# Performance work log

Measured on AMD Instinct MI355X. Metric: run time of the kernel, lower is better.

Reference implementation:

```python
import jax, jax.numpy as jnp
import numpy as np

NUM_VIEWS = 6
NUM_HEADS = 16
NUM_LAYERS = 2
DIST_THRESHOLD = 10.0
EPS = 1e-5


def layer_norm(x, g, b):
    m = jnp.mean(x, axis=-1, keepdims=True)
    v = jnp.mean((x - m) ** 2, axis=-1, keepdims=True)
    return (x - m) / jnp.sqrt(v + EPS) * g + b


def build_mask(coords3d, num_views, threshold):
    # coords3d: (B, T, 3) -> bool mask (B, T, T), True = masked
    B, T, _ = coords3d.shape
    tpv = T // num_views
    c = jnp.nan_to_num(coords3d, nan=0.0, posinf=100.0, neginf=-100.0)
    view_ids = jnp.repeat(jnp.arange(num_views), tpv)
    same_view = view_ids[:, None] == view_ids[None, :]  # (T, T)
    dist_sq = jnp.sum((c[:, :, None, :] - c[:, None, :, :]) ** 2, axis=-1)  # (B,T,T)
    mask = same_view[None] | (dist_sq > threshold * threshold)
    all_masked = jnp.all(mask, axis=-1)  # (B, T)
    eye = jnp.eye(T, dtype=bool)
    # unmask diagonal for rows that are fully masked (matches torch fix)
    mask = jnp.where(all_masked[:, :, None] & eye[None], False, mask)
    return mask


def mha(x, qkv_w, qkv_b, out_w, out_b, mask, num_heads):
    # x: (B,T,C); qkv_w: (3C,C); out_w: (C,C); mask: (B,T,T) True=masked
    B, T, C = x.shape
    hd = C // num_heads
    qkv = x @ qkv_w.T + qkv_b  # (B,T,3C)
    q, k, v = jnp.split(qkv, 3, axis=-1)
    def heads(t):
        return t.reshape(B, T, num_heads, hd).transpose(0, 2, 1, 3)  # (B,H,T,hd)
    q, k, v = heads(q), heads(k), heads(v)
    scale = 1.0 / jnp.sqrt(jnp.asarray(hd, x.dtype))
    scores = jnp.einsum('bhqd,bhkd->bhqk', q * scale, k)
    scores = jnp.where(mask[:, None], -jnp.inf, scores)
    attn = jax.nn.softmax(scores, axis=-1)
    o = jnp.einsum('bhqk,bhkd->bhqd', attn, v)  # (B,H,T,hd)
    o = o.transpose(0, 2, 1, 3).reshape(B, T, C)
    return o @ out_w.T + out_b


def setup_inputs() -> dict:
    key = jax.random.key(0)
    B, T, C, L = 2, 1536, 1024, NUM_LAYERS
    ks = jax.random.split(key, 16)
    s = 0.02
    inp = {
        'pos_embed': jax.random.normal(ks[0], (B, T, C), jnp.float32),
        'coords3d': jax.random.normal(ks[1], (B, T, 3), jnp.float32) * 8.0,
        'ln1_g': jnp.ones((L, C), jnp.float32),
        'ln1_b': jnp.zeros((L, C), jnp.float32),
        'qkv_w': jax.random.normal(ks[2], (L, 3 * C, C), jnp.float32) * s,
        'qkv_b': jnp.zeros((L, 3 * C), jnp.float32),
        'out_w': jax.random.normal(ks[3], (L, C, C), jnp.float32) * s,
        'out_b': jnp.zeros((L, C), jnp.float32),
        'ln2_g': jnp.ones((L, C), jnp.float32),
        'ln2_b': jnp.zeros((L, C), jnp.float32),
        'ffn_w1': jax.random.normal(ks[4], (L, 4 * C, C), jnp.float32) * s,
        'ffn_b1': jnp.zeros((L, 4 * C), jnp.float32),
        'ffn_w2': jax.random.normal(ks[5], (L, C, 4 * C), jnp.float32) * s,
        'ffn_b2': jnp.zeros((L, C), jnp.float32),
        'norm_g': jnp.ones((C,), jnp.float32),
        'norm_b': jnp.zeros((C,), jnp.float32),
    }
    return inp


def reference(pos_embed, coords3d, ln1_g, ln1_b, qkv_w, qkv_b, out_w, out_b,
              ln2_g, ln2_b, ffn_w1, ffn_b1, ffn_w2, ffn_b2, norm_g, norm_b):
    mask = build_mask(coords3d, NUM_VIEWS, DIST_THRESHOLD)
    x = pos_embed
    for l in range(NUM_LAYERS):
        xn = layer_norm(x, ln1_g[l], ln1_b[l])
        x = x + mha(xn, qkv_w[l], qkv_b[l], out_w[l], out_b[l], mask, NUM_HEADS)
        xn = layer_norm(x, ln2_g[l], ln2_b[l])
        h = jax.nn.gelu(xn @ ffn_w1[l].T + ffn_b1[l], approximate=False)
        x = x + (h @ ffn_w2[l].T + ffn_b2[l])
    return layer_norm(x, norm_g, norm_b)
```

## Files before the change

### kernel.cpp

```cpp
#include <hip/hip_runtime.h>

#define TT 1536
#define CC 1024
#define NH 16
#define HD 64
#define NL 2
#define NB 2
#define MM (NB*TT)

typedef unsigned short u16;
typedef unsigned int u32;
typedef unsigned long long u64;
typedef __attribute__((ext_vector_type(8))) short short8v;
typedef __attribute__((ext_vector_type(4))) float f32x4;

__device__ __forceinline__ u16 f2bf(float f){
  u32 u = __float_as_uint(f);
  u32 r = (u + 0x7FFFu + ((u >> 16) & 1u)) >> 16;
  return (u16)r;
}

__device__ __forceinline__ void gload_lds16(const void* g, void* l){
  __builtin_amdgcn_global_load_lds(
      (const __attribute__((address_space(1))) void*)g,
      (__attribute__((address_space(3))) void*)l, 16, 0, 0);
}

__device__ __forceinline__ f32x4 mfma16(short8v a, short8v b, f32x4 c){
  return __builtin_amdgcn_mfma_f32_16x16x32_bf16(a, b, c, 0, 0, 0);
}

__device__ __forceinline__ float exp2f_fast(float x){
  return __builtin_amdgcn_exp2f(x);
}

__device__ __forceinline__ u32 cvt_pk_bf16(float lo, float hi){
  u32 r;
  asm("v_cvt_pk_bf16_f32 %0, %1, %2" : "=v"(r) : "v"(lo), "v"(hi));
  return r;
}

__global__ __launch_bounds__(256) void cvt_bf16_kernel(const float* __restrict__ in,
                                                       u16* __restrict__ out, int n4){
  int stride = gridDim.x * 256;
  for (int i = blockIdx.x * 256 + threadIdx.x; i < n4; i += stride){
    const float4 v = ((const float4*)in)[i];
    ushort4 o;
    o.x = f2bf(v.x); o.y = f2bf(v.y); o.z = f2bf(v.z); o.w = f2bf(v.w);
    ((ushort4*)out)[i] = o;
  }
}

__device__ __forceinline__ float fixc(float v){
  if (__builtin_isnan(v)) return 0.0f;
  if (__builtin_isinf(v)) return v > 0.0f ? 100.0f : -100.0f;
  return v;
}

__global__ __launch_bounds__(256) void mask_kernel(const float* __restrict__ coords,
                                                   u64* __restrict__ maskw){
  const int tid = threadIdx.x, wave = tid >> 6, lane = tid & 63;
  const int ri = blockIdx.x * 4 + wave;
  const int b = ri / TT, i = ri - b * TT;
  const float* cp = coords + (size_t)ri * 3;
  const float cx = fixc(cp[0]), cy = fixc(cp[1]), cz = fixc(cp[2]);
  const int vi = i >> 8;
  u64 allm = ~0ull;
  for (int ch = 0; ch < 24; ++ch){
    const int j = ch * 64 + lane;
    const float* cj = coords + ((size_t)b * TT + j) * 3;
    const float dx = cx - fixc(cj[0]);
    const float dy = cy - fixc(cj[1]);
    const float dz = cz - fixc(cj[2]);
    const float d2 = dx*dx + dy*dy + dz*dz;
    const bool masked = ((j >> 8) == vi) || (d2 > 100.0f);
    const u64 bal = __ballot(masked);
    if (lane == 0) maskw[(size_t)ri * 24 + ch] = bal;
    allm &= bal;
  }
  if (lane == 0 && allm == ~0ull){
    const size_t w = (size_t)ri * 24 + (i >> 6);
    maskw[w] &= ~(1ull << (i & 63));
  }
}

template<int OUTF>
__global__ __launch_bounds__(256) void ln_kernel(const float* __restrict__ x,
    const float* __restrict__ gw, const float* __restrict__ bw,
    u16* __restrict__ outb, float* __restrict__ outf){
  __shared__ float sred[4];
  const int tid = threadIdx.x, wave = tid >> 6, lane = tid & 63;
  const size_t row = blockIdx.x;
  const float4 v = *(const float4*)(x + row * CC + tid * 4);
  float s = v.x + v.y + v.z + v.w;
  #pragma unroll
  for (int o = 1; o < 64; o <<= 1) s += __shfl_xor(s, o, 64);
  if (lane == 0) sred[wave] = s;
  __syncthreads();
  const float mean = (sred[0] + sred[1] + sred[2] + sred[3]) * (1.0f / CC);
  __syncthreads();
  const float d0 = v.x - mean, d1 = v.y - mean, d2 = v.z - mean, d3 = v.w - mean;
  float q = d0*d0 + d1*d1 + d2*d2 + d3*d3;
  #pragma unroll
  for (int o = 1; o < 64; o <<= 1) q += __shfl_xor(q, o, 64);
  if (lane == 0) sred[wave] = q;
  __syncthreads();
  const float var = (sred[0] + sred[1] + sred[2] + sred[3]) * (1.0f / CC);
  const float rstd = rsqrtf(var + 1e-5f);
  const float4 g4 = *(const float4*)(gw + tid * 4);
  const float4 b4 = *(const float4*)(bw + tid * 4);
  const float y0 = d0 * rstd * g4.x + b4.x;
  const float y1 = d1 * rstd * g4.y + b4.y;
  const float y2 = d2 * rstd * g4.z + b4.z;
  const float y3 = d3 * rstd * g4.w + b4.w;
  if (OUTF){
    *(float4*)(outf + row * CC + tid * 4) = make_float4(y0, y1, y2, y3);
  } else {
    ushort4 o4; o4.x = f2bf(y0); o4.y = f2bf(y1); o4.z = f2bf(y2); o4.w = f2bf(y3);
    *(ushort4*)(outb + row * CC + tid * 4) = o4;
  }
}

template<int EPI, int BM>
__global__ __launch_bounds__(512, 4) void gemm_nt(const u16* __restrict__ A,
    const u16* __restrict__ Bw, const float* __restrict__ bias,
    const float* __restrict__ res, u16* __restrict__ outb, float* __restrict__ outf,
    int M, int N, int K){
  __shared__ u16 As[2][BM][64];
  __shared__ u16 Bs[2][128][64];
  const int tid = threadIdx.x, wave = tid >> 6, lane = tid & 63;
  const int gx = gridDim.x;
  const int nwg = gx * gridDim.y;
  const int orig = blockIdx.y * gx + blockIdx.x;
  const int qq = nwg >> 3, rm = nwg & 7;
  const int xcd = orig & 7, pos = orig >> 3;
  const int wg = (xcd < rm ? xcd * (qq + 1) : rm * (qq + 1) + (xcd - rm) * qq) + pos;
  const int m0 = (wg / gx) * BM, n0 = (wg % gx) * 128;
  constexpr int NFR = (BM == 128) ? 4 : 2;
  constexpr int CW = 16 * NFR;
  const int wr = (BM == 128) ? (wave >> 1) : (wave >> 2);
  const int wc = (BM == 128) ? (wave & 1) : (wave & 3);
  f32x4 acc[2][NFR];
  #pragma unroll
  for (int mi = 0; mi < 2; ++mi)
    #pragma unroll
    for (int ni = 0; ni < NFR; ++ni){ f32x4 z = {0.f,0.f,0.f,0.f}; acc[mi][ni] = z; }

  const u16* Ag = A + (size_t)m0 * K;
  const u16* Bg = Bw + (size_t)n0 * K;
  const int srow0 = wave * 8 + (lane >> 3);
  const int scole = ((lane & 7) ^ (lane >> 3)) * 8;
  auto stage = [&](int buf, int k0){
    char* ab = (char*)&As[buf][0][0];
    char* bb = (char*)&Bs[buf][0][0];
    #pragma unroll
    for (int l = 0; l < BM/64; ++l)
      gload_lds16(Ag + (size_t)(l*64 + srow0) * K + k0 + scole, ab + (l*8 + wave) * 1024);
    #pragma unroll
    for (int l = 0; l < 2; ++l)
      gload_lds16(Bg + (size_t)(l*64 + srow0) * K + k0 + scole, bb + (l*8 + wave) * 1024);
  };

  const int NT = K >> 6;
  stage(0, 0);
  stage(1, 64);

  const int ar = lane & 15, akb = (lane >> 4) * 16;
  const int rsw = (ar & 7) << 4;
  for (int t = 0; t < NT; ++t){
    const int cur = t & 1;
    if (t + 1 < NT){
      if constexpr (BM == 128) asm volatile("s_waitcnt vmcnt(4)" ::: "memory");
      else                     asm volatile("s_waitcnt vmcnt(3)" ::: "memory");
    } else {
      asm volatile("s_waitcnt vmcnt(0)" ::: "memory");
    }
    __builtin_amdgcn_s_barrier();
    const char* ab = (const char*)&As[cur][0][0];
    const char* bb = (const char*)&Bs[cur][0][0];
    short8v af[2][2], bf[NFR][2];
    #pragma unroll
    for (int ks = 0; ks < 2; ++ks){
      const int cb = (ks*64 + akb) ^ rsw;
      #pragma unroll
      for (int mi = 0; mi < 2; ++mi)
        af[mi][ks] = *(const short8v*)(ab + (wr*32 + mi*16 + ar)*128 + cb);
      #pragma unroll
      for (int ni = 0; ni < NFR; ++ni)
        bf[ni][ks] = *(const short8v*)(bb + (wc*CW + ni*16 + ar)*128 + cb);
    }
    asm volatile("s_waitcnt lgkmcnt(0)" ::: "memory");
    __builtin_amdgcn_sched_barrier(0);
    __builtin_amdgcn_s_barrier();
    if (t + 2 < NT) stage(cur, (t + 2) * 64);
    __builtin_amdgcn_s_setprio(1);
    #pragma unroll
    for (int ks = 0; ks < 2; ++ks)
      #pragma unroll
      for (int mi = 0; mi < 2; ++mi)
        #pragma unroll
        for (int ni = 0; ni < NFR; ++ni)
          acc[mi][ni] = mfma16(af[mi][ks], bf[ni][ks], acc[mi][ni]);
    __builtin_amdgcn_s_setprio(0);
  }

  const int cr = (lane >> 4) * 4, cl = lane & 15;
  #pragma unroll
  for (int ni = 0; ni < NFR; ++ni){
    const int c = n0 + wc*CW + ni*16 + cl;
    const float bv = bias[c];
    #pragma unroll
    for (int mi = 0; mi < 2; ++mi){
      #pragma unroll
      for (int r = 0; r < 4; ++r){
        const size_t rr2 = (size_t)(m0 + wr*32 + mi*16 + cr + r);
        float v = acc[mi][ni][r] + bv;
        if constexpr (EPI == 1) v = 0.5f * v * (1.0f + erff(v * 0.70710678118654752f));
        if constexpr (EPI == 2) outf[rr2 * N + c] = v + res[rr2 * N + c];
        else outb[rr2 * N + c] = f2bf(v);
      }
    }
  }
}

__global__ __launch_bounds__(256, 3) void attn_kernel(const u16* __restrict__ qkv,
    const u64* __restrict__ maskw, u16* __restrict__ outp){
  __shared__ u16 Ks[2][64][64];
  __shared__ u16 Vt[2][64][64];
  __shared__ u16 Ps[4][16][64];
  const int tid = threadIdx.x, wave = tid >> 6, lane = tid & 63;
  const int nwgA = gridDim.x * gridDim.y;
  const int flatA = blockIdx.y * gridDim.x + blockIdx.x;
  const int virt = (flatA & 7) * (nwgA >> 3) + (flatA >> 3);
  const int bh = virt / (TT/64);
  const int qt = virt - bh * (TT/64);
  const int b = bh >> 4, h = bh & 15;
  const int qb = qt * 64;
  const int rs = 3 * CC;
  const int g4 = lane >> 4;
  const int l15 = lane & 15;
  const int qrow = qb + wave * 16 + l15;
  const u16* kv_base = qkv + (size_t)b * TT * rs;

  const float qscale = 0.18033688011112042f;
  const u16* qp = kv_base + (size_t)qrow * rs + h * HD + g4 * 8;
  short8v qf0, qf1;
  {
    const short8v r0 = *(const short8v*)qp;
    const short8v r1 = *(const short8v*)(qp + 32);
    #pragma unroll
    for (int e = 0; e < 8; ++e){
      qf0[e] = (short)f2bf(__uint_as_float(((u32)(u16)r0[e]) << 16) * qscale);
      qf1[e] = (short)f2bf(__uint_as_float(((u32)(u16)r1[e]) << 16) * qscale);
    }
  }

  f32x4 o[4], lacc;
  #pragma unroll
  for (int dt = 0; dt < 4; ++dt){ f32x4 z = {0.f,0.f,0.f,0.f}; o[dt] = z; }
  { f32x4 z = {0.f,0.f,0.f,0.f}; lacc = z; }
  float m_r = -1.0e4f;

  const int sw = (l15 & 7) << 4;
  const int swl = (lane & 7) << 4;
  int koff[4][2], voff[4][2], pwoff[4], proff[2], vwoff[2];
  #pragma unroll
  for (int jt = 0; jt < 4; ++jt){
    koff[jt][0] = (jt*16 + l15)*128 + ((g4*16) ^ sw);
    koff[jt][1] = (jt*16 + l15)*128 + ((64 + g4*16) ^ sw);
    voff[jt][0] = koff[jt][0];
    voff[jt][1] = koff[jt][1];
    pwoff[jt] = wave*2048 + l15*128 + ((jt*32 + g4*8) ^ sw);
  }
  proff[0] = wave*2048 + l15*128 + ((g4*16) ^ sw);
  proff[1] = wave*2048 + l15*128 + ((64 + g4*16) ^ sw);
  vwoff[0] = lane*128 + ((wave*16) ^ swl);
  vwoff[1] = lane*128 + ((64 + wave*16) ^ swl);

  const int scol = CC + h * HD + (((lane & 7) ^ (lane >> 3)) * 8);
  const u16* skp0 = kv_base + (size_t)(64 + wave*16 + (lane >> 3)) * rs + scol;
  const u16* skp1 = skp0 + 8 * rs;
  const u16* vp   = kv_base + (size_t)(64 + wave*8) * rs + 2*CC + h*HD + lane;
  const u64* mp2  = maskw + (size_t)(b * TT + qrow) * 24;

  char* KsB = (char*)&Ks[0][0][0];
  char* VtB = (char*)&Vt[0][0][0];
  char* PsB = (char*)&Ps[0][0][0];

  short8v vone;
  #pragma unroll
  for (int e = 0; e < 8; ++e) vone[e] = (short)0x3F80;

  {
    u16 vv[16];
    #pragma unroll
    for (int e = 0; e < 8; ++e)
      vv[e] = kv_base[(size_t)(wave*8 + e) * rs + 2*CC + h*HD + lane];
    #pragma unroll
    for (int e = 0; e < 8; ++e)
      vv[8+e] = kv_base[(size_t)(32 + wave*8 + e) * rs + 2*CC + h*HD + lane];
    gload_lds16(kv_base + (size_t)(wave*16 + (lane>>3)) * rs + scol,
                KsB + (wave*2 + 0) * 1024);
    gload_lds16(kv_base + (size_t)(wave*16 + 8 + (lane>>3)) * rs + scol,
                KsB + (wave*2 + 1) * 1024);
    short8v sv0, sv1;
    #pragma unroll
    for (int e = 0; e < 8; ++e){ sv0[e] = (short)vv[e]; sv1[e] = (short)vv[8+e]; }
    *(short8v*)(VtB + vwoff[0]) = sv0;
    *(short8v*)(VtB + vwoff[1]) = sv1;
    __syncthreads();
  }

  auto chunk = [&](int buf, bool pf){
    u16 vv[16];
    if (pf){
      #pragma unroll
      for (int e = 0; e < 8; ++e) vv[e] = vp[(size_t)e * rs];
      #pragma unroll
      for (int e = 0; e < 8; ++e) vv[8+e] = vp[(size_t)(32 + e) * rs];
      gload_lds16(skp0, KsB + (buf^1)*8192 + (wave*2 + 0)*1024);
      gload_lds16(skp1, KsB + (buf^1)*8192 + (wave*2 + 1)*1024);
    }
    const u64 mw = mp2[buf];
    const u32 mwlo = (u32)mw, mwhi = (u32)(mw >> 32);

    const char* Kb = KsB + buf * 8192;
    f32x4 S[4];
    #pragma unroll
    for (int jt = 0; jt < 4; ++jt){
      const short8v k0 = *(const short8v*)(Kb + koff[jt][0]);
      const short8v k1 = *(const short8v*)(Kb + koff[jt][1]);
      f32x4 z = {0.f,0.f,0.f,0.f};
      z = mfma16(k0, qf0, z);
      z = mfma16(k1, qf1, z);
      S[jt] = z;
    }

    float ps[16];
    float cmax = -3.0e38f;
    #pragma unroll
    for (int jt = 0; jt < 4; ++jt){
      const u32 msrc = (jt & 2) ? mwhi : mwlo;
      const int sh = g4 * 4 + (jt & 1) * 16;
      #pragma unroll
      for (int r = 0; r < 4; ++r){
        float s = S[jt][r];
        s = ((msrc >> (sh + r)) & 1u) ? -3.0e38f : s;
        ps[jt*4+r] = s;
        cmax = fmaxf(cmax, s);
      }
    }
    cmax = fmaxf(cmax, __shfl_xor(cmax, 16));
    cmax = fmaxf(cmax, __shfl_xor(cmax, 32));

    if (!__all(cmax <= m_r + 8.0f)){
      const float mnew = fmaxf(m_r, cmax);
      const float fac = exp2f_fast(m_r - mnew);
      m_r = mnew;
      float fr4[4];
      #pragma unroll
      for (int r = 0; r < 4; ++r) fr4[r] = __shfl(fac, g4 * 4 + r);
      #pragma unroll
      for (int dt = 0; dt < 4; ++dt){
        f32x4 tt = o[dt];
        tt[0] *= fr4[0]; tt[1] *= fr4[1]; tt[2] *= fr4[2]; tt[3] *= fr4[3];
        o[dt] = tt;
      }
      lacc[0] *= fr4[0]; lacc[1] *= fr4[1]; lacc[2] *= fr4[2]; lacc[3] *= fr4[3];
    }

    #pragma unroll
    for (int i = 0; i < 16; ++i) ps[i] = exp2f_fast(ps[i] - m_r);

    #pragma unroll
    for (int jt = 0; jt < 4; ++jt){
      uint2 pk;
      pk.x = cvt_pk_bf16(ps[jt*4+0], ps[jt*4+1]);
      pk.y = cvt_pk_bf16(ps[jt*4+2], ps[jt*4+3]);
      *(uint2*)(PsB + pwoff[jt]) = pk;
    }

    short8v pA[2];
    pA[0] = *(const short8v*)(PsB + proff[0]);
    pA[1] = *(const short8v*)(PsB + proff[1]);
    const char* Vb = VtB + buf * 8192;
    __builtin_amdgcn_s_setprio(1);
    #pragma unroll
    for (int dt = 0; dt < 4; ++dt){
      #pragma unroll
      for (int kc = 0; kc < 2; ++kc){
        const short8v vf = *(const short8v*)(Vb + voff[dt][kc]);
        o[dt] = mfma16(pA[kc], vf, o[dt]);
      }
    }
    lacc = mfma16(pA[0], vone, lacc);
    lacc = mfma16(pA[1], vone, lacc);
    __builtin_amdgcn_s_setprio(0);

    if (pf){
      short8v sv0, sv1;
      #pragma unroll
      for (int e = 0; e < 8; ++e){ sv0[e] = (short)vv[e]; sv1[e] = (short)vv[8+e]; }
      char* Vd = VtB + (buf^1) * 8192;
      *(short8v*)(Vd + vwoff[0]) = sv0;
      *(short8v*)(Vd + vwoff[1]) = sv1;
      vp += (size_t)64 * rs; skp0 += (size_t)64 * rs; skp1 += (size_t)64 * rs;
    }
    __syncthreads();
  };

  for (int th = 0; th < 12; ++th){
    chunk(0, true);
    chunk(1, th < 11);
    mp2 += 2;
  }

  float linv[4];
  #pragma unroll
  for (int r = 0; r < 4; ++r) linv[r] = 1.0f / fmaxf(lacc[r], 1e-30f);
  #pragma unroll
  for (int dt = 0; dt < 4; ++dt)
    #pragma unroll
    for (int r = 0; r < 4; ++r)
      outp[(size_t)(b * TT + qb + wave * 16 + g4 * 4 + r) * CC + h * HD + dt * 16 + l15] =
          f2bf(o[dt][r] * linv[r]);
}

extern "C" void kernel_launch(void* const* d_in, const int* in_sizes, int n_in,
                              void* d_out, int out_size, void* d_ws, size_t ws_size,
                              hipStream_t stream){
  (void)in_sizes; (void)n_in; (void)out_size; (void)ws_size;
  const float* pos    = (const float*)d_in[0];
  const float* coords = (const float*)d_in[1];
  const float* ln1g   = (const float*)d_in[2];
  const float* ln1b   = (const float*)d_in[3];
  const float* qkvw   = (const float*)d_in[4];
  const float* qkvbi  = (const float*)d_in[5];
  const float* outw   = (const float*)d_in[6];
  const float* outbi  = (const float*)d_in[7];
  const float* ln2g   = (const float*)d_in[8];
  const float* ln2b   = (const float*)d_in[9];
  const float* w1     = (const float*)d_in[10];
  const float* b1     = (const float*)d_in[11];
  const float* w2     = (const float*)d_in[12];
  const float* b2     = (const float*)d_in[13];
  const float* ng     = (const float*)d_in[14];
  const float* nbb    = (const float*)d_in[15];

  char* wsp = (char*)d_ws;
  size_t off = 0;
  auto alloc = [&](size_t bytes)->void*{
    void* p = wsp + off; off += (bytes + 255) & ~(size_t)255; return p;
  };
  u16* qkvw_bf = (u16*)alloc((size_t)NL*3*CC*CC*sizeof(u16));
  u16* outw_bf = (u16*)alloc((size_t)NL*CC*CC*sizeof(u16));
  u16* w1_bf   = (u16*)alloc((size_t)NL*4*CC*CC*sizeof(u16));
  u16* w2_bf   = (u16*)alloc((size_t)NL*4*CC*CC*sizeof(u16));
  float* x     = (float*)alloc((size_t)MM*CC*sizeof(float));
  u16* xn      = (u16*)alloc((size_t)MM*CC*sizeof(u16));
  u16* qkvbuf  = (u16*)alloc((size_t)MM*4*CC*sizeof(u16));
  u16* attnb   = (u16*)alloc((size_t)MM*CC*sizeof(u16));
  u64* maskw   = (u64*)alloc((size_t)MM*24*sizeof(u64));
  u16* hbuf = qkvbuf;

  auto cvt = [&](const float* s, u16* dst, size_t n){
    int n4 = (int)(n >> 2);
    int blocks = (n4 + 255) / 256; if (blocks > 4096) blocks = 4096;
    cvt_bf16_kernel<<<dim3(blocks), dim3(256), 0, stream>>>(s, dst, n4);
  };
  cvt(qkvw, qkvw_bf, (size_t)NL*3*CC*CC);
  cvt(outw, outw_bf, (size_t)NL*CC*CC);
  cvt(w1, w1_bf, (size_t)NL*4*CC*CC);
  cvt(w2, w2_bf, (size_t)NL*4*CC*CC);

  hipMemcpyAsync(x, pos, (size_t)MM*CC*sizeof(float), hipMemcpyDeviceToDevice, stream);
  mask_kernel<<<dim3(MM/4), dim3(256), 0, stream>>>(coords, maskw);

  for (int l = 0; l < NL; ++l){
    ln_kernel<0><<<dim3(MM), dim3(256), 0, stream>>>(x, ln1g + l*CC, ln1b + l*CC, xn, nullptr);
    gemm_nt<0,128><<<dim3(3*CC/128, MM/128), dim3(512), 0, stream>>>(
        xn, qkvw_bf + (size_t)l*3*CC*CC, qkvbi + l*3*CC, nullptr, qkvbuf, nullptr, MM, 3*CC, CC);
    attn_kernel<<<dim3(TT/64, NB*NH), dim3(256), 0, stream>>>(qkvbuf, maskw, attnb);
    gemm_nt<2,64><<<dim3(CC/128, MM/64), dim3(512), 0, stream>>>(
        attnb, outw_bf + (size_t)l*CC*CC, outbi + l*CC, x, nullptr, x, MM, CC, CC);
    ln_kernel<0><<<dim3(MM), dim3(256), 0, stream>>>(x, ln2g + l*CC, ln2b + l*CC, xn, nullptr);
    gemm_nt<1,128><<<dim3(4*CC/128, MM/128), dim3(512), 0, stream>>>(
        xn, w1_bf + (size_t)l*4*CC*CC, b1 + l*4*CC, nullptr, hbuf, nullptr, MM, 4*CC, CC);
    gemm_nt<2,64><<<dim3(CC/128, MM/64), dim3(512), 0, stream>>>(
        hbuf, w2_bf + (size_t)l*4*CC*CC, b2 + l*CC, x, nullptr, x, MM, CC, 4*CC);
  }
  ln_kernel<1><<<dim3(MM), dim3(256), 0, stream>>>(x, ng, nbb, nullptr, (float*)d_out);
}
```

Baseline: 425.6 us.

## Add 4-wave 128x128 GEMM with 64x64 per-wave tiles for QKV and FFN1

Adds a 256-thread GEMM variant in which each of four waves computes a 64x64 sub-tile (4x4 MFMA fragments) instead of the 8-wave layout, and uses it for the QKV projection and the first FFN GEMM. The larger per-wave tile raises register-level reuse of the A and B fragments loaded from LDS, cutting LDS read traffic per MFMA. The cost is more accumulator registers and lower occupancy (launch bounds of 2 blocks). The attention kernel's launch bound is also raised from 3 to 4 blocks per CU, which pushes its register budget down and may cause spills.

```diff
diff --git a/kernel.cpp b/kernel.cpp
--- a/kernel.cpp
+++ b/kernel.cpp
@@ -121,6 +121,100 @@
   }
 }
 
+template<int EPI>
+__global__ __launch_bounds__(256, 2) void gemm_nt4(const u16* __restrict__ A,
+    const u16* __restrict__ Bw, const float* __restrict__ bias,
+    const float* __restrict__ res, u16* __restrict__ outb, float* __restrict__ outf,
+    int M, int N, int K){
+  __shared__ u16 As[2][128][64];
+  __shared__ u16 Bs[2][128][64];
+  const int tid = threadIdx.x, wave = tid >> 6, lane = tid & 63;
+  const int gx = gridDim.x;
+  const int nwg = gx * gridDim.y;
+  const int orig = blockIdx.y * gx + blockIdx.x;
+  const int qq = nwg >> 3, rm = nwg & 7;
+  const int xcd = orig & 7, pos = orig >> 3;
+  const int wg = (xcd < rm ? xcd * (qq + 1) : rm * (qq + 1) + (xcd - rm) * qq) + pos;
+  const int m0 = (wg / gx) * 128, n0 = (wg % gx) * 128;
+  const int wr = wave >> 1, wc = wave & 1;
+  f32x4 acc[4][4];
+  #pragma unroll
+  for (int mi = 0; mi < 4; ++mi)
+    #pragma unroll
+    for (int ni = 0; ni < 4; ++ni){ f32x4 z = {0.f,0.f,0.f,0.f}; acc[mi][ni] = z; }
+
+  const u16* Ag = A + (size_t)m0 * K;
+  const u16* Bg = Bw + (size_t)n0 * K;
+  const int srow0 = tid >> 3;
+  const int scole = ((tid & 7) ^ ((tid >> 3) & 7)) * 8;
+  auto stage = [&](int buf, int k0){
+    char* ab = (char*)&As[buf][0][0];
+    char* bb = (char*)&Bs[buf][0][0];
+    #pragma unroll
+    for (int l = 0; l < 4; ++l){
+      gload_lds16(Ag + (size_t)(l*32 + srow0) * K + k0 + scole, ab + l*4096 + tid*16);
+      gload_lds16(Bg + (size_t)(l*32 + srow0) * K + k0 + scole, bb + l*4096 + tid*16);
+    }
+  };
+
+  const int NT = K >> 6;
+  stage(0, 0);
+  stage(1, 64);
+
+  const int ar = lane & 15, akb = (lane >> 4) * 16;
+  const int rsw = (ar & 7) << 4;
+  for (int t = 0; t < NT; ++t){
+    const int cur = t & 1;
+    if (t + 1 < NT) asm volatile("s_waitcnt vmcnt(8)" ::: "memory");
+    else            asm volatile("s_waitcnt vmcnt(0)" ::: "memory");
+    __builtin_amdgcn_s_barrier();
+    const char* ab = (const char*)&As[cur][0][0];
+    const char* bb = (const char*)&Bs[cur][0][0];
+    short8v af[4][2], bf[4][2];
+    #pragma unroll
+    for (int ks = 0; ks < 2; ++ks){
+      const int cb = (ks*64 + akb) ^ rsw;
+      #pragma unroll
+      for (int mi = 0; mi < 4; ++mi)
+        af[mi][ks] = *(const short8v*)(ab + (wr*64 + mi*16 + ar)*128 + cb);
+      #pragma unroll
+      for (int ni = 0; ni < 4; ++ni)
+        bf[ni][ks] = *(const short8v*)(bb + (wc*64 + ni*16 + ar)*128 + cb);
+    }
+    asm volatile("s_waitcnt lgkmcnt(0)" ::: "memory");
+    __builtin_amdgcn_sched_barrier(0);
+    __builtin_amdgcn_s_barrier();
+    if (t + 2 < NT) stage(cur, (t + 2) * 64);
+    __builtin_amdgcn_s_setprio(1);
+    #pragma unroll
+    for (int ks = 0; ks < 2; ++ks)
+      #pragma unroll
+      for (int mi = 0; mi < 4; ++mi)
+        #pragma unroll
+        for (int ni = 0; ni < 4; ++ni)
+          acc[mi][ni] = mfma16(af[mi][ks], bf[ni][ks], acc[mi][ni]);
+    __builtin_amdgcn_s_setprio(0);
+  }
+
+  const int cr = (lane >> 4) * 4, cl = lane & 15;
+  #pragma unroll
+  for (int ni = 0; ni < 4; ++ni){
+    const int c = n0 + wc*64 + ni*16 + cl;
+    const float bv = bias[c];
+    #pragma unroll
+    for (int mi = 0; mi < 4; ++mi){
+      #pragma unroll
+      for (int r = 0; r < 4; ++r){
+        const size_t rr2 = (size_t)(m0 + wr*64 + mi*16 + cr + r);
+        float v = acc[mi][ni][r] + bv;
+        if constexpr (EPI == 1) v = 0.5f * v * (1.0f + erff(v * 0.70710678118654752f));
+        if constexpr (EPI == 2) outf[rr2 * N + c] = v + res[rr2 * N + c];
+        else outb[rr2 * N + c] = f2bf(v);
+      }
+    }
+  }
+}
+
 template<int EPI, int BM>
 __global__ __launch_bounds__(512, 4) void gemm_nt(const u16* __restrict__ A,
     const u16* __restrict__ Bw, const float* __restrict__ bias,
@@ -223,7 +317,7 @@
   }
 }
 
-__global__ __launch_bounds__(256, 3) void attn_kernel(const u16* __restrict__ qkv,
+__global__ __launch_bounds__(256, 4) void attn_kernel(const u16* __restrict__ qkv,
     const u64* __restrict__ maskw, u16* __restrict__ outp){
   __shared__ u16 Ks[2][64][64];
   __shared__ u16 Vt[2][64][64];
@@ -478,13 +572,13 @@
 
   for (int l = 0; l < NL; ++l){
     ln_kernel<0><<<dim3(MM), dim3(256), 0, stream>>>(x, ln1g + l*CC, ln1b + l*CC, xn, nullptr);
-    gemm_nt<0,128><<<dim3(3*CC/128, MM/128), dim3(512), 0, stream>>>(
+    gemm_nt4<0><<<dim3(3*CC/128, MM/128), dim3(256), 0, stream>>>(
         xn, qkvw_bf + (size_t)l*3*CC*CC, qkvbi + l*3*CC, nullptr, qkvbuf, nullptr, MM, 3*CC, CC);
     attn_kernel<<<dim3(TT/64, NB*NH), dim3(256), 0, stream>>>(qkvbuf, maskw, attnb);
     gemm_nt<2,64><<<dim3(CC/128, MM/64), dim3(512), 0, stream>>>(
         attnb, outw_bf + (size_t)l*CC*CC, outbi + l*CC, x, nullptr, x, MM, CC, CC);
     ln_kernel<0><<<dim3(MM), dim3(256), 0, stream>>>(x, ln2g + l*CC, ln2b + l*CC, xn, nullptr);
-    gemm_nt<1,128><<<dim3(4*CC/128, MM/128), dim3(512), 0, stream>>>(
+    gemm_nt4<1><<<dim3(4*CC/128, MM/128), dim3(256), 0, stream>>>(
         xn, w1_bf + (size_t)l*4*CC*CC, b1 + l*4*CC, nullptr, hbuf, nullptr, MM, 4*CC, CC);
     gemm_nt<2,64><<<dim3(CC/128, MM/64), dim3(512), 0, stream>>>(
         hbuf, w2_bf + (size_t)l*4*CC*CC, b2 + l*CC, x, nullptr, x, MM, CC, 4*CC);
```

Measured after the change: 442.7 us. 4.0% more time.

## Store residual stream in bf16 and raise attention occupancy bound

Applied to the files above, without the earlier changes.

The fp32 residual stream x becomes bf16. LayerNorm reads bf16, and the residual GEMM epilogues read and write bf16 instead of fp32. The initial device copy of pos_embed becomes a bf16 conversion kernel. This halves residual read/write traffic in the LN and projection epilogues, at the cost of accumulating rounding error in the residual across layers. The attention kernel's launch bounds also change from 3 to 4 waves-per-SIMD minimum, which may increase register pressure or spills.

```diff
diff --git a/kernel.cpp b/kernel.cpp
--- a/kernel.cpp
+++ b/kernel.cpp
@@ -18,6 +18,10 @@
   u32 u = __float_as_uint(f);
   u32 r = (u + 0x7FFFu + ((u >> 16) & 1u)) >> 16;
   return (u16)r;
+}
+
+__device__ __forceinline__ float b2f(u16 u){
+  return __uint_as_float(((u32)u) << 16);
 }
 
 __device__ __forceinline__ void gload_lds16(const void* g, void* l){
@@ -85,21 +89,22 @@
 }
 
 template<int OUTF>
-__global__ __launch_bounds__(256) void ln_kernel(const float* __restrict__ x,
+__global__ __launch_bounds__(256) void ln_kernel(const u16* __restrict__ x,
     const float* __restrict__ gw, const float* __restrict__ bw,
     u16* __restrict__ outb, float* __restrict__ outf){
   __shared__ float sred[4];
   const int tid = threadIdx.x, wave = tid >> 6, lane = tid & 63;
   const size_t row = blockIdx.x;
-  const float4 v = *(const float4*)(x + row * CC + tid * 4);
-  float s = v.x + v.y + v.z + v.w;
+  const ushort4 vu = *(const ushort4*)(x + row * CC + tid * 4);
+  const float v0 = b2f(vu.x), v1 = b2f(vu.y), v2 = b2f(vu.z), v3 = b2f(vu.w);
+  float s = v0 + v1 + v2 + v3;
   #pragma unroll
   for (int o = 1; o < 64; o <<= 1) s += __shfl_xor(s, o, 64);
   if (lane == 0) sred[wave] = s;
   __syncthreads();
   const float mean = (sred[0] + sred[1] + sred[2] + sred[3]) * (1.0f / CC);
   __syncthreads();
-  const float d0 = v.x - mean, d1 = v.y - mean, d2 = v.z - mean, d3 = v.w - mean;
+  const float d0 = v0 - mean, d1 = v1 - mean, d2 = v2 - mean, d3 = v3 - mean;
   float q = d0*d0 + d1*d1 + d2*d2 + d3*d3;
   #pragma unroll
   for (int o = 1; o < 64; o <<= 1) q += __shfl_xor(q, o, 64);
@@ -124,7 +129,7 @@
 template<int EPI, int BM>
 __global__ __launch_bounds__(512, 4) void gemm_nt(const u16* __restrict__ A,
     const u16* __restrict__ Bw, const float* __restrict__ bias,
-    const float* __restrict__ res, u16* __restrict__ outb, float* __restrict__ outf,
+    const u16* __restrict__ res, u16* __restrict__ outb,
     int M, int N, int K){
   __shared__ u16 As[2][BM][64];
   __shared__ u16 Bs[2][128][64];
@@ -216,14 +221,14 @@
         const size_t rr2 = (size_t)(m0 + wr*32 + mi*16 + cr + r);
         float v = acc[mi][ni][r] + bv;
         if constexpr (EPI == 1) v = 0.5f * v * (1.0f + erff(v * 0.70710678118654752f));
-        if constexpr (EPI == 2) outf[rr2 * N + c] = v + res[rr2 * N + c];
-        else outb[rr2 * N + c] = f2bf(v);
+        if constexpr (EPI == 2) v += b2f(res[rr2 * N + c]);
+        outb[rr2 * N + c] = f2bf(v);
       }
     }
   }
 }
 
-__global__ __launch_bounds__(256, 3) void attn_kernel(const u16* __restrict__ qkv,
+__global__ __launch_bounds__(256, 4) void attn_kernel(const u16* __restrict__ qkv,
     const u64* __restrict__ maskw, u16* __restrict__ outp){
   __shared__ u16 Ks[2][64][64];
   __shared__ u16 Vt[2][64][64];
@@ -250,8 +255,8 @@
     const short8v r1 = *(const short8v*)(qp + 32);
     #pragma unroll
     for (int e = 0; e < 8; ++e){
-      qf0[e] = (short)f2bf(__uint_as_float(((u32)(u16)r0[e]) << 16) * qscale);
-      qf1[e] = (short)f2bf(__uint_as_float(((u32)(u16)r1[e]) << 16) * qscale);
+      qf0[e] = (short)f2bf(b2f((u16)r0[e]) * qscale);
+      qf1[e] = (short)f2bf(b2f((u16)r1[e]) * qscale);
     }
   }
 
@@ -456,7 +461,7 @@
   u16* outw_bf = (u16*)alloc((size_t)NL*CC*CC*sizeof(u16));
   u16* w1_bf   = (u16*)alloc((size_t)NL*4*CC*CC*sizeof(u16));
   u16* w2_bf   = (u16*)alloc((size_t)NL*4*CC*CC*sizeof(u16));
-  float* x     = (float*)alloc((size_t)MM*CC*sizeof(float));
+  u16* x       = (u16*)alloc((size_t)MM*CC*sizeof(u16));
   u16* xn      = (u16*)alloc((size_t)MM*CC*sizeof(u16));
   u16* qkvbuf  = (u16*)alloc((size_t)MM*4*CC*sizeof(u16));
   u16* attnb   = (u16*)alloc((size_t)MM*CC*sizeof(u16));
@@ -472,22 +477,22 @@
   cvt(outw, outw_bf, (size_t)NL*CC*CC);
   cvt(w1, w1_bf, (size_t)NL*4*CC*CC);
   cvt(w2, w2_bf, (size_t)NL*4*CC*CC);
-
-  hipMemcpyAsync(x, pos, (size_t)MM*CC*sizeof(float), hipMemcpyDeviceToDevice, stream);
+  cvt(pos, x, (size_t)MM*CC);
+
   mask_kernel<<<dim3(MM/4), dim3(256), 0, stream>>>(coords, maskw);
 
   for (int l = 0; l < NL; ++l){
     ln_kernel<0><<<dim3(MM), dim3(256), 0, stream>>>(x, ln1g + l*CC, ln1b + l*CC, xn, nullptr);
     gemm_nt<0,128><<<dim3(3*CC/128, MM/128), dim3(512), 0, stream>>>(
-        xn, qkvw_bf + (size_t)l*3*CC*CC, qkvbi + l*3*CC, nullptr, qkvbuf, nullptr, MM, 3*CC, CC);
+        xn, qkvw_bf + (size_t)l*3*CC*CC, qkvbi + l*3*CC, nullptr, qkvbuf, MM, 3*CC, CC);
     attn_kernel<<<dim3(TT/64, NB*NH), dim3(256), 0, stream>>>(qkvbuf, maskw, attnb);
     gemm_nt<2,64><<<dim3(CC/128, MM/64), dim3(512), 0, stream>>>(
-        attnb, outw_bf + (size_t)l*CC*CC, outbi + l*CC, x, nullptr, x, MM, CC, CC);
+        attnb, outw_bf + (size_t)l*CC*CC, outbi + l*CC, x, x, MM, CC, CC);
     ln_kernel<0><<<dim3(MM), dim3(256), 0, stream>>>(x, ln2g + l*CC, ln2b + l*CC, xn, nullptr);
     gemm_nt<1,128><<<dim3(4*CC/128, MM/128), dim3(512), 0, stream>>>(
-        xn, w1_bf + (size_t)l*4*CC*CC, b1 + l*4*CC, nullptr, hbuf, nullptr, MM, 4*CC, CC);
+        xn, w1_bf + (size_t)l*4*CC*CC, b1 + l*4*CC, nullptr, hbuf, MM, 4*CC, CC);
     gemm_nt<2,64><<<dim3(CC/128, MM/64), dim3(512), 0, stream>>>(
-        hbuf, w2_bf + (size_t)l*4*CC*CC, b2 + l*CC, x, nullptr, x, MM, CC, 4*CC);
+        hbuf, w2_bf + (size_t)l*4*CC*CC, b2 + l*CC, x, x, MM, CC, 4*CC);
   }
   ln_kernel<1><<<dim3(MM), dim3(256), 0, stream>>>(x, ng, nbb, nullptr, (float*)d_out);
 }
```

Result: no change. 419.2 us (-1.5%).
